# Kernel optimization log

Hardware: AMD Instinct MI355X
Metric: run time of the kernel (lower is better)

## Reference

```python
import jax, jax.numpy as jnp
import numpy as np

THRESH = 0.5  # best_threshold from get_best_t('greedy-t', opts)


def setup_inputs() -> dict:
    key = jax.random.key(0)
    B, V, U1 = 4096, 128, 129  # batch, v_size (arriving nodes), u_size + 1 (skip slot at col 0)
    w = jax.random.uniform(key, (B, V, U1), dtype=jnp.float32)
    w = w.at[:, :, 0].set(0.0)  # skip action has zero weight
    return {"weights": w}


def _decode(weights, t):
    # weights: [B, V, U1]; sequential greedy-threshold decoding over the V arriving nodes.
    B, V, U1 = weights.shape

    def step(carry, w_i):
        mask, size = carry            # mask: [B, U1] bool (matched u nodes), size: [B]
        w = jnp.where(mask, 0.0, w_i)  # w[mask] = 0
        w = jnp.where(w < t, 0.0, w)   # threshold: zero weights below t
        fallback = w.sum(axis=1) == 0.0
        w = w.at[:, 0].set(jnp.where(fallback, 1.0, w[:, 0]))  # force skip if nothing passes
        sel = jnp.argmax(w, axis=1)    # [B]
        chosen = jnp.take_along_axis(w_i, sel[:, None], axis=1)[:, 0]  # original edge weight
        onehot = jax.nn.one_hot(sel, U1, dtype=bool).at[:, 0].set(False)  # skip never masked
        return (mask | onehot, size + chosen), sel

    init = (jnp.zeros((B, U1), dtype=bool), jnp.zeros((B,), weights.dtype))
    (mask, size), sels = jax.lax.scan(step, init, jnp.swapaxes(weights, 0, 1))
    # returns (-state.size, sequences) as in the torch module (return_pi=False path)
    return -size, jnp.swapaxes(sels, 0, 1)


def reference(weights):
    return _decode(weights, THRESH)
```

## Files before the change

### kernel.cpp

```cpp
#include <hip/hip_runtime.h>


#define NB 4096
#define NV 128
#define NU1 129
#define WPB 4
#define PD 8

__device__ __forceinline__ unsigned mkkey(float v, unsigned inv) {
    unsigned k = ((__float_as_uint(v) & 0x7FFFFFu) << 8) | inv;
    return v >= 0.5f ? k : 0u;
}

#define DPPMAX(x, ctl)                                                         \
    asm("s_nop 1\n\tv_max_i32_dpp %0, %0, %0 " ctl                             \
        " row_mask:0xf bank_mask:0xf"                                          \
        : "+v"(x))

__global__ __launch_bounds__(256)
void greedy_thresh_kernel(const float* __restrict__ w, float* __restrict__ out) {
    const int wave = blockIdx.x * WPB + (threadIdx.x >> 6);
    const int lane = threadIdx.x & 63;

    const float* __restrict__ wb = w + (size_t)wave * (NV * NU1);
    float* __restrict__ out_neg = out;
    float* __restrict__ out_sel = out + NB;

    const int c0 = 1 + lane;
    const int c1 = 65 + lane;
    const unsigned inv0 = 255 - c0;
    const unsigned inv1 = 255 - c1;
    unsigned keep0 = ~0u, keep1 = ~0u;
    float size = 0.0f;
    float s0 = 0.0f, s1 = 0.0f;

    float p0[PD], p1[PD];
    #pragma unroll
    for (int d = 0; d < PD; ++d) {
        p0[d] = wb[d * NU1 + c0];
        p1[d] = wb[d * NU1 + c1];
    }
    unsigned kr0 = mkkey(p0[0], inv0);
    unsigned kr1 = mkkey(p1[0], inv1);

#define BODY(iexpr, dd, PREF, BLD)                                             \
    {                                                                          \
        const int i = (iexpr);                                                 \
                                                \
        unsigned ka = kr0 & keep0;                                             \
        unsigned kb = kr1 & keep1;                                             \
        int v = (int)(ka > kb ? ka : kb);                                      \
                                \
        if (PREF) {                                                            \
            const float* nrow = wb + (size_t)(i + PD) * NU1;                   \
            p0[dd] = nrow[c0];                                                 \
            p1[dd] = nrow[c1];                                                 \
        }                                                                      \
                                    \
        if (BLD) {                                                             \
            kr0 = mkkey(p0[(dd + 1) & (PD - 1)], inv0);                        \
            kr1 = mkkey(p1[(dd + 1) & (PD - 1)], inv1);                        \
        }                                                                      \
                          \
        DPPMAX(v, "row_shr:1");                                                \
        DPPMAX(v, "row_shr:2");                                                \
        DPPMAX(v, "row_shr:4");                                                \
        DPPMAX(v, "row_shr:8");                                                \
        DPPMAX(v, "row_bcast:15");                                             \
        DPPMAX(v, "row_bcast:31");                                             \
        unsigned kk;                                                           \
        asm("s_nop 1\n\tv_readlane_b32 %0, %1, 63" : "=s"(kk) : "v"(v));       \
                                                   \
        const int sel = kk ? (255 - (int)(kk & 0xFFu)) : 0;                    \
        size += __uint_as_float(kk ? (0x3F000000u | (kk >> 8)) : 0u);          \
        keep0 = (sel == c0) ? 0u : keep0;                                      \
        keep1 = (sel == c1) ? 0u : keep1;                                      \
        const float self = (float)sel;                                         \
        if ((i >> 1) == lane) { if (i & 1) s1 = self; else s0 = self; }        \
    }

    for (int ib = 0; ib < NV - PD; ib += PD) {
        #pragma unroll
        for (int d = 0; d < PD; ++d)
            BODY(ib + d, d, true, true)
    }
    #pragma unroll
    for (int d = 0; d < PD; ++d)
        BODY(NV - PD + d, d, false, (d < PD - 1))

#undef BODY

    float2 sv = make_float2(s0, s1);
    *reinterpret_cast<float2*>(&out_sel[(size_t)wave * NV + 2 * lane]) = sv;
    if (lane == 0) out_neg[wave] = -size;
}

extern "C" void kernel_launch(void* const* d_in, const int* in_sizes, int n_in,
                              void* d_out, int out_size, void* d_ws, size_t ws_size,
                              hipStream_t stream) {
    const float* w = (const float*)d_in[0];
    float* out = (float*)d_out;
    const int blocks = NB / WPB;
    greedy_thresh_kernel<<<blocks, 64 * WPB, 0, stream>>>(w, out);
}
```

Before: 47.84 us.

## Deepen row prefetch and replace inline-asm DPP reduction with builtins

Doubles the prefetch depth of weight rows from 8 to 16, giving more loads in flight per wave at the cost of extra registers. Swaps the hand-written DPP max asm for __builtin_amdgcn_update_dpp plus readlane so the compiler can schedule the required hazard waits instead of fixed s_nop padding. The mask update now compares each lane's key to the reduced key rather than recomputing the selected column, and the key no longer masks off the exponent bits. Selection indices are kept as ints until the final store.

```diff
diff --git a/kernel.cpp b/kernel.cpp
--- a/kernel.cpp
+++ b/kernel.cpp
@@ -5,17 +5,16 @@
 #define NV 128
 #define NU1 129
 #define WPB 4
-#define PD 8
+#define PD 16
 
 __device__ __forceinline__ unsigned mkkey(float v, unsigned inv) {
-    unsigned k = ((__float_as_uint(v) & 0x7FFFFFu) << 8) | inv;
+    unsigned k = (__float_as_uint(v) << 8) | inv;
     return v >= 0.5f ? k : 0u;
 }
 
-#define DPPMAX(x, ctl)                                                         \
-    asm("s_nop 1\n\tv_max_i32_dpp %0, %0, %0 " ctl                             \
-        " row_mask:0xf bank_mask:0xf"                                          \
-        : "+v"(x))
+#define DPPSTAGE(v, ctl)                                                       \
+    { int _t = __builtin_amdgcn_update_dpp(0, v, ctl, 0xf, 0xf, true);         \
+      v = v > _t ? v : _t; }
 
 __global__ __launch_bounds__(256)
 void greedy_thresh_kernel(const float* __restrict__ w, float* __restrict__ out) {
@@ -30,9 +29,10 @@
     const int c1 = 65 + lane;
     const unsigned inv0 = 255 - c0;
     const unsigned inv1 = 255 - c1;
-    unsigned keep0 = ~0u, keep1 = ~0u;
+
+    unsigned kp0 = ~0u, kp1 = ~0u;
     float size = 0.0f;
-    float s0 = 0.0f, s1 = 0.0f;
+    int s0 = 0, s1 = 0;
 
     float p0[PD], p1[PD];
     #pragma unroll
@@ -46,37 +46,32 @@
 #define BODY(iexpr, dd, PREF, BLD)                                             \
     {                                                                          \
         const int i = (iexpr);                                                 \
-                                                \
-        unsigned ka = kr0 & keep0;                                             \
-        unsigned kb = kr1 & keep1;                                             \
-        int v = (int)(ka > kb ? ka : kb);                                      \
-                                \
+        const unsigned a0 = kr0 & kp0;                                         \
+        const unsigned a1 = kr1 & kp1;                                         \
+        int v = (int)(a0 > a1 ? a0 : a1);                                      \
         if (PREF) {                                                            \
             const float* nrow = wb + (size_t)(i + PD) * NU1;                   \
             p0[dd] = nrow[c0];                                                 \
             p1[dd] = nrow[c1];                                                 \
         }                                                                      \
-                                    \
         if (BLD) {                                                             \
             kr0 = mkkey(p0[(dd + 1) & (PD - 1)], inv0);                        \
             kr1 = mkkey(p1[(dd + 1) & (PD - 1)], inv1);                        \
         }                                                                      \
-                          \
-        DPPMAX(v, "row_shr:1");                                                \
-        DPPMAX(v, "row_shr:2");                                                \
-        DPPMAX(v, "row_shr:4");                                                \
-        DPPMAX(v, "row_shr:8");                                                \
-        DPPMAX(v, "row_bcast:15");                                             \
-        DPPMAX(v, "row_bcast:31");                                             \
-        unsigned kk;                                                           \
-        asm("s_nop 1\n\tv_readlane_b32 %0, %1, 63" : "=s"(kk) : "v"(v));       \
-                                                   \
+        DPPSTAGE(v, 0x111)                                     \
+        DPPSTAGE(v, 0x112)                                     \
+        DPPSTAGE(v, 0x114)                                     \
+        DPPSTAGE(v, 0x118)                                     \
+        DPPSTAGE(v, 0x142)                                   \
+        DPPSTAGE(v, 0x143)                                   \
+        const unsigned kk = (unsigned)__builtin_amdgcn_readlane(v, 63);        \
+        const unsigned cv = kk ? kk : ~0u;     \
+        kp0 = (a0 == cv) ? 0u : kp0;                                           \
+        kp1 = (a1 == cv) ? 0u : kp1;                                           \
+            \
+        size += __uint_as_float(kk ? (0x3F000000u | (kk >> 8)) : 0u);          \
         const int sel = kk ? (255 - (int)(kk & 0xFFu)) : 0;                    \
-        size += __uint_as_float(kk ? (0x3F000000u | (kk >> 8)) : 0u);          \
-        keep0 = (sel == c0) ? 0u : keep0;                                      \
-        keep1 = (sel == c1) ? 0u : keep1;                                      \
-        const float self = (float)sel;                                         \
-        if ((i >> 1) == lane) { if (i & 1) s1 = self; else s0 = self; }        \
+        if ((i >> 1) == lane) { if (i & 1) s1 = sel; else s0 = sel; }          \
     }
 
     for (int ib = 0; ib < NV - PD; ib += PD) {
@@ -90,8 +85,8 @@
 
 #undef BODY
 
-    float2 sv = make_float2(s0, s1);
-    *reinterpret_cast<float2*>(&out_sel[(size_t)wave * NV + 2 * lane]) = sv;
+    *reinterpret_cast<float2*>(&out_sel[(size_t)wave * NV + 2 * lane]) =
+        make_float2((float)s0, (float)s1);
     if (lane == 0) out_neg[wave] = -size;
 }
 
```

New measurement: 50.79 us. +6.2%, slower.
